# Kernel optimization log

Measured on AMD Instinct MI355X. Metric: run time of the kernel, lower is better.

## Reference

```python
import jax, jax.numpy as jnp
import numpy as np
import math

M = 0.5
S = 64.0
COS_M = math.cos(M)
SIN_M = math.sin(M)
THRESHOLD = math.cos(math.pi - M)
MM = math.sin(math.pi - M) * M

B, D, N_CLASSES = 512, 512, 100000


def setup_inputs() -> dict:
    key = jax.random.key(0)
    k1, k2, k3 = jax.random.split(key, 3)
    embeddings = jax.random.normal(k1, (B, D), dtype=jnp.float32)
    labels = jax.random.randint(k2, (B,), 0, N_CLASSES, dtype=jnp.int32)
    kernel = jax.random.normal(k3, (D, N_CLASSES), dtype=jnp.float32) * 0.05
    t = jnp.zeros((), dtype=jnp.float32)
    return {"embeddings": embeddings, "labels": labels, "kernel": kernel, "t": t}


def reference(embeddings, labels, kernel, t):
    # L2 normalize embeddings (rows) and kernel (columns)
    emb = embeddings / jnp.linalg.norm(embeddings, axis=1, keepdims=True)
    kn = kernel / jnp.linalg.norm(kernel, axis=0, keepdims=True)
    cos_theta = jnp.clip(emb @ kn, -1.0, 1.0)  # [B, C]

    b = cos_theta.shape[0]
    rows = jnp.arange(b)
    target_logit = cos_theta[rows, labels][:, None]  # [B, 1]
    sin_theta = jnp.sqrt(1.0 - jnp.square(target_logit))
    cos_theta_m = target_logit * COS_M - sin_theta * SIN_M  # [B, 1]

    mask = cos_theta > cos_theta_m  # [B, C] hard examples
    final_target_logit = jnp.where(target_logit > THRESHOLD,
                                   cos_theta_m, target_logit - MM)  # [B, 1]

    # EMA update of t (assigned before the hard-example scaling in TF code)
    new_t = 0.01 * jnp.mean(target_logit) + 0.99 * t

    # hard examples: c -> c * (t + c); others unchanged
    cos_theta = jnp.where(mask, cos_theta * (new_t + cos_theta), cos_theta)
    # overwrite label column with the margin-adjusted target logit
    cos_theta = cos_theta.at[rows, labels].set(final_target_logit[:, 0])
    return cos_theta * S
```

## Files before the change

### kernel.cpp

```cpp
#include <hip/hip_runtime.h>
#include <hip/hip_bf16.h>
#include <cstdint>
#include <cstddef>

#define C_N 100000
#define B_N 512
#define D_N 512

#define COS_M_F   0.87758256189037276f
#define SIN_M_F   0.47942553860420301f
#define THRESH_F  (-0.87758256189037276f)
#define MM_F      0.23971276930210150f
#define S_F       64.0f

typedef __attribute__((ext_vector_type(8))) short short8;
typedef __attribute__((ext_vector_type(4))) float f32x4;

__device__ __forceinline__ unsigned short f2bf(float f) {
  unsigned u = __float_as_uint(f);
  u = u + 0x7fffu + ((u >> 16) & 1u);
  return (unsigned short)(u >> 16);
}

__device__ __forceinline__ float wave_sum(float v) {
#pragma unroll
  for (int o = 32; o > 0; o >>= 1) v += __shfl_down(v, o, 64);
  return v;
}

__device__ __forceinline__ void lds_load16(const void* g, void* l) {
  __builtin_amdgcn_global_load_lds(
      (const __attribute__((address_space(1))) unsigned int*)g,
      (__attribute__((address_space(3))) unsigned int*)l, 16, 0, 0);
}

__launch_bounds__(512)
__global__ void knorm2_k(const float* __restrict__ Kp, float* __restrict__ cninv,
                         unsigned short* __restrict__ Knt) {
  __shared__ __align__(16) unsigned short Tl[64 * 512];
  __shared__ float ssum[32][64];
  __shared__ float cns[64];

  const int t = threadIdx.x;
  const int j0 = blockIdx.x * 64;
  const int jq = t & 15;
  const int dr = t >> 4;
  const int jcol = min((j0 >> 2) + jq, (C_N >> 2) - 1);
  const float4* __restrict__ Kv = (const float4*)Kp;

  float4 v[16];
#pragma unroll
  for (int i = 0; i < 16; ++i)
    v[i] = Kv[(size_t)(dr * 16 + i) * (C_N / 4) + jcol];

  float s0 = 0.f, s1 = 0.f, s2 = 0.f, s3 = 0.f;
#pragma unroll
  for (int i = 0; i < 16; ++i) {
    s0 = fmaf(v[i].x, v[i].x, s0);
    s1 = fmaf(v[i].y, v[i].y, s1);
    s2 = fmaf(v[i].z, v[i].z, s2);
    s3 = fmaf(v[i].w, v[i].w, s3);
  }
  ssum[dr][jq * 4 + 0] = s0;
  ssum[dr][jq * 4 + 1] = s1;
  ssum[dr][jq * 4 + 2] = s2;
  ssum[dr][jq * 4 + 3] = s3;
  __syncthreads();
  if (t < 64) {
    float s = 0.f;
#pragma unroll
    for (int d = 0; d < 32; ++d) s += ssum[d][t];
    float r = rsqrtf(fmaxf(s, 1e-30f));
    cns[t] = r;
    if (j0 + t < C_N) cninv[j0 + t] = r;
  }
  __syncthreads();

  const float r0 = cns[jq * 4 + 0];
  const float r1 = cns[jq * 4 + 1];
  const float r2 = cns[jq * 4 + 2];
  const float r3 = cns[jq * 4 + 3];
#pragma unroll
  for (int g = 0; g < 4; ++g) {
    const int ch = dr * 2 + (g >> 1);
    const int sub = (g & 1) * 8;
#pragma unroll
    for (int c = 0; c < 4; ++c) {
      const int j = jq * 4 + c;
      const float rc = (c == 0) ? r0 : (c == 1) ? r1 : (c == 2) ? r2 : r3;
      unsigned lo, hi;
      lo = (unsigned)f2bf(v[g * 4 + 0][c] * rc) | ((unsigned)f2bf(v[g * 4 + 1][c] * rc) << 16);
      hi = (unsigned)f2bf(v[g * 4 + 2][c] * rc) | ((unsigned)f2bf(v[g * 4 + 3][c] * rc) << 16);
      const int phys = ch ^ (j & 7);
      *(uint2*)((char*)Tl + j * 1024 + phys * 16 + sub) = make_uint2(lo, hi);
    }
  }
  __syncthreads();

  const int jr = t >> 3;
  const int dc = t & 7;
  const int jg = j0 + jr;
  if (jg < C_N) {
#pragma unroll
    for (int s = 0; s < 8; ++s) {
      const int phys = (s * 8) + (dc ^ (jr & 7));
      uint4 val = *(const uint4*)((const char*)Tl + jr * 1024 + phys * 16);
      *(uint4*)(&Knt[(size_t)jg * D_N + s * 64 + dc * 8]) = val;
    }
  }
}

__global__ void embnorm_k(const float* __restrict__ emb, unsigned short* __restrict__ embn,
                          float* __restrict__ rinv) {
  int row = blockIdx.x;
  int t = threadIdx.x;
  float4 v = ((const float4*)(emb + (size_t)row * D_N))[t];
  float ss = v.x * v.x + v.y * v.y + v.z * v.z + v.w * v.w;
  ss = wave_sum(ss);
  __shared__ float red[2];
  if ((t & 63) == 0) red[t >> 6] = ss;
  __syncthreads();
  float tot = red[0] + red[1];
  float ri = rsqrtf(tot);
  if (t == 0) rinv[row] = ri;
  ushort4 o;
  o.x = f2bf(v.x * ri); o.y = f2bf(v.y * ri); o.z = f2bf(v.z * ri); o.w = f2bf(v.w * ri);
  ((ushort4*)(embn + (size_t)row * D_N))[t] = o;
}

__global__ void target2_k(const float* __restrict__ emb, const float* __restrict__ Kp,
                          const float* __restrict__ rinv, const int* __restrict__ labels,
                          float* __restrict__ target, float* __restrict__ ctm,
                          float* __restrict__ ft) {
  int row = blockIdx.x;
  int t = threadIdx.x;
  int lab = labels[row];
  float p = 0.f, ss = 0.f;
  for (int d = t; d < D_N; d += 256) {
    float kv = Kp[(size_t)d * C_N + lab];
    p = fmaf(emb[(size_t)row * D_N + d], kv, p);
    ss = fmaf(kv, kv, ss);
  }
  p = wave_sum(p);
  ss = wave_sum(ss);
  __shared__ float redp[4], reds[4];
  if ((t & 63) == 0) { redp[t >> 6] = p; reds[t >> 6] = ss; }
  __syncthreads();
  if (t == 0) {
    float dot = redp[0] + redp[1] + redp[2] + redp[3];
    float sums = reds[0] + reds[1] + reds[2] + reds[3];
    float tg = dot * rinv[row] * rsqrtf(fmaxf(sums, 1e-30f));
    tg = fminf(fmaxf(tg, -1.f), 1.f);
    float st = sqrtf(fmaxf(1.f - tg * tg, 0.f));
    float cm = tg * COS_M_F - st * SIN_M_F;
    float f = (tg > THRESH_F) ? cm : (tg - MM_F);
    target[row] = tg;
    ctm[row] = cm;
    ft[row] = f;
  }
}

__global__ void newt_k(const float* __restrict__ target, const float* __restrict__ t_in,
                       float* __restrict__ newt) {
  int t = threadIdx.x;
  float v = target[t];
  v = wave_sum(v);
  __shared__ float red[8];
  if ((t & 63) == 0) red[t >> 6] = v;
  __syncthreads();
  if (t == 0) {
    float s = 0.f;
#pragma unroll
    for (int i = 0; i < 8; ++i) s += red[i];
    *newt = 0.01f * (s / (float)B_N) + 0.99f * t_in[0];
  }
}

__launch_bounds__(1024, 4)
__global__ void gemm8_k(const unsigned short* __restrict__ Knt,
                        const unsigned short* __restrict__ embn,
                        const int* __restrict__ labels,
                        const float* __restrict__ ctm, const float* __restrict__ ft,
                        const float* __restrict__ newt_p, float* __restrict__ out) {
  __shared__ __align__(16) char lds[81920];
  unsigned short* Al = (unsigned short*)lds;
  unsigned short* Bb = (unsigned short*)(lds + 65536);

  const int t = threadIdx.x;
  const int l = t & 63, w = t >> 6;
  const int j0 = blockIdx.x * 128;

  const int sidx = (l & 7) ^ (l >> 3);
  const int r0 = ((l >> 3) << 1) | (sidx >> 2);
  const int kc8 = (sidx & 3) * 8;

  const unsigned short* asrc = embn + (size_t)(w * 32 + r0) * D_N + kc8;
  const unsigned short* bsrc = Knt + (size_t)(j0 + (w & 7) * 16 + r0) * D_N + kc8;

#pragma unroll
  for (int p = 0; p < 2; ++p)
    lds_load16(asrc + p * 16 * D_N, Al + w * 1024 + p * 512);
  if (w < 8) lds_load16(bsrc, Bb + w * 512);
  __syncthreads();

  const int wr = w >> 2, wc = w & 3;
  const int lq = l >> 4, lr = l & 15;
  const int s16 = ((((lr & 1) << 2) | lq) ^ (lr >> 1)) << 4;
  const int rh = lr >> 1;

  f32x4 acc[8][2];
#pragma unroll
  for (int mb = 0; mb < 8; ++mb) {
    acc[mb][0] = 0;
    acc[mb][1] = 0;
  }

#pragma unroll
  for (int it = 0; it < 16; ++it) {
    const int cur = it & 1, nxt = cur ^ 1;
    if (it < 15) {
      const int k0 = (it + 1) * 32;
#pragma unroll
      for (int p = 0; p < 2; ++p)
        lds_load16(asrc + p * 16 * D_N + k0, Al + nxt * 16384 + w * 1024 + p * 512);
      if (w < 8) lds_load16(bsrc + k0, Bb + nxt * 4096 + w * 512);
    }
    const char* Ab = (const char*)(Al + cur * 16384);
    const char* Bt = (const char*)(Bb + cur * 4096);
    short8 b0 = *(const short8*)(Bt + ((wc * 16 + 0 + rh) << 7) + s16);
    short8 b1 = *(const short8*)(Bt + ((wc * 16 + 8 + rh) << 7) + s16);
#pragma unroll
    for (int mb = 0; mb < 8; ++mb) {
      short8 a = *(const short8*)(Ab + ((wr * 64 + mb * 8 + rh) << 7) + s16);
      acc[mb][0] = __builtin_amdgcn_mfma_f32_16x16x32_bf16(a, b0, acc[mb][0], 0, 0, 0);
      acc[mb][1] = __builtin_amdgcn_mfma_f32_16x16x32_bf16(a, b1, acc[mb][1], 0, 0, 0);
    }
    __syncthreads();
  }

  const float newt = *newt_p;
  float* Tl = (float*)lds;
  const int row_l = t >> 3;
  const int sgl = t & 7;
  const int rx = row_l & 7;

#pragma unroll
  for (int pp = 0; pp < 4; ++pp) {
    if (wr == pp) {
#pragma unroll
      for (int mb = 0; mb < 8; ++mb) {
#pragma unroll
        for (int nb = 0; nb < 2; ++nb) {
          const int seg = nb * 4 + (lr >> 2);
          const int e = lr & 3;
#pragma unroll
          for (int r = 0; r < 4; ++r) {
            const int rl = mb * 16 + lq * 4 + r;
            const int ps = seg ^ (rl & 7);
            Tl[rl * 128 + wc * 32 + ps * 4 + e] = acc[mb][nb][r];
          }
        }
      }
    }
    __syncthreads();
    const int grow = pp * 128 + row_l;
    const int lab = labels[grow];
    const float cm = ctm[grow];
    const float f = ft[grow];
#pragma unroll
    for (int k = 0; k < 4; ++k) {
      const int jb = j0 + k * 32 + sgl * 4;
      if (jb < C_N) {
        f32x4 vv = *(const f32x4*)&Tl[row_l * 128 + k * 32 + (sgl ^ rx) * 4];
#pragma unroll
        for (int e = 0; e < 4; ++e) {
          float c = fminf(fmaxf(vv[e], -1.f), 1.f);
          float o = (c > cm) ? c * (newt + c) : c;
          o = (jb + e == lab) ? f : o;
          vv[e] = o * S_F;
        }
        *(f32x4*)&out[(size_t)grow * C_N + jb] = vv;
      }
    }
    __syncthreads();
  }
}

extern "C" void kernel_launch(void* const* d_in, const int* in_sizes, int n_in,
                              void* d_out, int out_size, void* d_ws, size_t ws_size,
                              hipStream_t stream) {
  (void)in_sizes; (void)n_in; (void)out_size; (void)ws_size;
  const float* emb = (const float*)d_in[0];
  const int* labels = (const int*)d_in[1];
  const float* Kp = (const float*)d_in[2];
  const float* t_in = (const float*)d_in[3];
  float* out = (float*)d_out;

  char* wsp = (char*)d_ws;
  const size_t KNT_BYTES = (size_t)100096 * D_N * 2;
  unsigned short* Knt = (unsigned short*)(wsp + 0);
  unsigned short* embn = (unsigned short*)(wsp + KNT_BYTES);
  float* cninv  = (float*)(wsp + KNT_BYTES + 524288);
  float* target = (float*)(wsp + KNT_BYTES + 524288 + 400000);
  float* ctm    = (float*)(wsp + KNT_BYTES + 524288 + 400000 + 2048);
  float* ft     = (float*)(wsp + KNT_BYTES + 524288 + 400000 + 2 * 2048);
  float* rinv   = (float*)(wsp + KNT_BYTES + 524288 + 400000 + 3 * 2048);
  float* newt   = (float*)(wsp + KNT_BYTES + 524288 + 400000 + 4 * 2048);

  knorm2_k<<<(C_N + 63) / 64, 512, 0, stream>>>(Kp, cninv, Knt);
  embnorm_k<<<B_N, 128, 0, stream>>>(emb, embn, rinv);
  target2_k<<<B_N, 256, 0, stream>>>(emb, Kp, rinv, labels, target, ctm, ft);
  newt_k<<<1, 512, 0, stream>>>(target, t_in, newt);
  gemm8_k<<<(C_N + 127) / 128, 1024, 0, stream>>>(Knt, embn, labels, ctm, ft, newt, out);
}
```

Measured before the change: 201.2 us.

## Remap GEMM blocks per XCD and pipeline global-to-LDS loads with explicit waitcnts

Block indices are remapped so consecutive column tiles land on the same XCD, which should improve L2 locality for the shared embedding tile. The K loop now issues two stages ahead and replaces __syncthreads with explicit vmcnt/lgkmcnt waits and raw s_barrier, so global loads can overlap MFMA work instead of draining every iteration. It relies on hand-counted outstanding-load counts, which become wrong if lds_load16's instruction count changes.

```diff
diff --git a/kernel.cpp b/kernel.cpp
--- a/kernel.cpp
+++ b/kernel.cpp
@@ -177,7 +177,7 @@
 }
 
 __launch_bounds__(1024, 4)
-__global__ void gemm8_k(const unsigned short* __restrict__ Knt,
+__global__ void gemm9_k(const unsigned short* __restrict__ Knt,
                         const unsigned short* __restrict__ embn,
                         const int* __restrict__ labels,
                         const float* __restrict__ ctm, const float* __restrict__ ft,
@@ -188,7 +188,12 @@
 
   const int t = threadIdx.x;
   const int l = t & 63, w = t >> 6;
-  const int j0 = blockIdx.x * 128;
+
+  const int nwg = gridDim.x;
+  const int q = nwg >> 3, r = nwg & 7;
+  const int xcd = blockIdx.x & 7, seq = blockIdx.x >> 3;
+  const int wg = (xcd < r ? xcd * (q + 1) : r * (q + 1) + (xcd - r) * q) + seq;
+  const int j0 = wg * 128;
 
   const int sidx = (l & 7) ^ (l >> 3);
   const int r0 = ((l >> 3) << 1) | (sidx >> 2);
@@ -197,11 +202,16 @@
   const unsigned short* asrc = embn + (size_t)(w * 32 + r0) * D_N + kc8;
   const unsigned short* bsrc = Knt + (size_t)(j0 + (w & 7) * 16 + r0) * D_N + kc8;
 
-#pragma unroll
-  for (int p = 0; p < 2; ++p)
-    lds_load16(asrc + p * 16 * D_N, Al + w * 1024 + p * 512);
-  if (w < 8) lds_load16(bsrc, Bb + w * 512);
-  __syncthreads();
+#define STAGE9(it, buf)                                                        \
+  do {                                                                         \
+    const int k0_ = (it) * 32;                                                 \
+    lds_load16(asrc + k0_, Al + (buf) * 16384 + w * 1024);                     \
+    lds_load16(asrc + 16 * D_N + k0_, Al + (buf) * 16384 + w * 1024 + 512);    \
+    if (w < 8) lds_load16(bsrc + k0_, Bb + (buf) * 4096 + w * 512);            \
+  } while (0)
+
+  STAGE9(0, 0);
+  STAGE9(1, 1);
 
   const int wr = w >> 2, wc = w & 3;
   const int lq = l >> 4, lr = l & 15;
@@ -217,14 +227,19 @@
 
 #pragma unroll
   for (int it = 0; it < 16; ++it) {
-    const int cur = it & 1, nxt = cur ^ 1;
-    if (it < 15) {
-      const int k0 = (it + 1) * 32;
-#pragma unroll
-      for (int p = 0; p < 2; ++p)
-        lds_load16(asrc + p * 16 * D_N + k0, Al + nxt * 16384 + w * 1024 + p * 512);
-      if (w < 8) lds_load16(bsrc + k0, Bb + nxt * 4096 + w * 512);
-    }
+    const int cur = it & 1;
+    if (it >= 1 && it < 15) STAGE9(it + 1, cur ^ 1);
+    if (it == 15) {
+      asm volatile("s_waitcnt vmcnt(0)" ::: "memory");
+    } else if (w < 8) {
+      asm volatile("s_waitcnt vmcnt(3)" ::: "memory");
+    } else {
+      asm volatile("s_waitcnt vmcnt(2)" ::: "memory");
+    }
+    __builtin_amdgcn_sched_barrier(0);
+    __builtin_amdgcn_s_barrier();
+    __builtin_amdgcn_sched_barrier(0);
+
     const char* Ab = (const char*)(Al + cur * 16384);
     const char* Bt = (const char*)(Bb + cur * 4096);
     short8 b0 = *(const short8*)(Bt + ((wc * 16 + 0 + rh) << 7) + s16);
@@ -235,8 +250,12 @@
       acc[mb][0] = __builtin_amdgcn_mfma_f32_16x16x32_bf16(a, b0, acc[mb][0], 0, 0, 0);
       acc[mb][1] = __builtin_amdgcn_mfma_f32_16x16x32_bf16(a, b1, acc[mb][1], 0, 0, 0);
     }
-    __syncthreads();
-  }
+    asm volatile("s_waitcnt lgkmcnt(0)" ::: "memory");
+    __builtin_amdgcn_sched_barrier(0);
+    __builtin_amdgcn_s_barrier();
+    __builtin_amdgcn_sched_barrier(0);
+  }
+#undef STAGE9
 
   const float newt = *newt_p;
   float* Tl = (float*)lds;
@@ -254,10 +273,10 @@
           const int seg = nb * 4 + (lr >> 2);
           const int e = lr & 3;
 #pragma unroll
-          for (int r = 0; r < 4; ++r) {
-            const int rl = mb * 16 + lq * 4 + r;
+          for (int rr = 0; rr < 4; ++rr) {
+            const int rl = mb * 16 + lq * 4 + rr;
             const int ps = seg ^ (rl & 7);
-            Tl[rl * 128 + wc * 32 + ps * 4 + e] = acc[mb][nb][r];
+            Tl[rl * 128 + wc * 32 + ps * 4 + e] = acc[mb][nb][rr];
           }
         }
       }
@@ -311,5 +330,5 @@
   embnorm_k<<<B_N, 128, 0, stream>>>(emb, embn, rinv);
   target2_k<<<B_N, 256, 0, stream>>>(emb, Kp, rinv, labels, target, ctm, ft);
   newt_k<<<1, 512, 0, stream>>>(target, t_in, newt);
-  gemm8_k<<<(C_N + 127) / 128, 1024, 0, stream>>>(Knt, embn, labels, ctm, ft, newt, out);
-}
+  gemm9_k<<<(C_N + 127) / 128, 1024, 0, stream>>>(Knt, embn, labels, ctm, ft, newt, out);
+}
```

After: 201.9 us. No clear change (+0.4%).

## Retile GEMM to 256x64 blocks with direct epilogue stores

Applied to the files above, without the earlier changes.

Replaces the 1024-thread kernel (512 rows x 128 columns per block) with 256-thread blocks that each cover 256 rows x 64 columns, giving more, smaller blocks with a smaller LDS footprint per block. The epilogue no longer stages results through LDS for coalesced float4 stores. Each lane now writes scalar floats straight from its MFMA accumulators. This drops the LDS transpose and its barriers, but the global stores become strided and scalar, which may hurt write coalescing on a store-bound output. Each embedding tile is also reloaded once per column tile.

```diff
diff --git a/kernel.cpp b/kernel.cpp
--- a/kernel.cpp
+++ b/kernel.cpp
@@ -176,34 +176,36 @@
   }
 }
 
-__launch_bounds__(1024, 4)
-__global__ void gemm8_k(const unsigned short* __restrict__ Knt,
-                        const unsigned short* __restrict__ embn,
-                        const int* __restrict__ labels,
-                        const float* __restrict__ ctm, const float* __restrict__ ft,
-                        const float* __restrict__ newt_p, float* __restrict__ out) {
-  __shared__ __align__(16) char lds[81920];
-  unsigned short* Al = (unsigned short*)lds;
-  unsigned short* Bb = (unsigned short*)(lds + 65536);
+__launch_bounds__(256, 4)
+__global__ void gemm10_k(const unsigned short* __restrict__ Knt,
+                         const unsigned short* __restrict__ embn,
+                         const int* __restrict__ labels,
+                         const float* __restrict__ ctm, const float* __restrict__ ft,
+                         const float* __restrict__ newt_p, float* __restrict__ out) {
+  __shared__ __align__(16) unsigned short Al[2][8192];
+  __shared__ __align__(16) unsigned short Bb[2][2048];
 
   const int t = threadIdx.x;
   const int l = t & 63, w = t >> 6;
-  const int j0 = blockIdx.x * 128;
+  const int mi = blockIdx.x & 1;
+  const int jb = blockIdx.x >> 1;
+  const int m0 = mi * 256;
+  const int j0 = jb * 64;
 
   const int sidx = (l & 7) ^ (l >> 3);
   const int r0 = ((l >> 3) << 1) | (sidx >> 2);
   const int kc8 = (sidx & 3) * 8;
 
-  const unsigned short* asrc = embn + (size_t)(w * 32 + r0) * D_N + kc8;
-  const unsigned short* bsrc = Knt + (size_t)(j0 + (w & 7) * 16 + r0) * D_N + kc8;
-
-#pragma unroll
-  for (int p = 0; p < 2; ++p)
-    lds_load16(asrc + p * 16 * D_N, Al + w * 1024 + p * 512);
-  if (w < 8) lds_load16(bsrc, Bb + w * 512);
-  __syncthreads();
-
-  const int wr = w >> 2, wc = w & 3;
+  const unsigned short* asrc = embn + (size_t)(m0 + w * 64 + r0) * D_N + kc8;
+  const unsigned short* bsrc = Knt + (size_t)(j0 + w * 16 + r0) * D_N + kc8;
+
+#pragma unroll
+  for (int p = 0; p < 4; ++p)
+    lds_load16(asrc + p * 16 * D_N, &Al[0][w * 2048 + p * 512]);
+  lds_load16(bsrc, &Bb[0][w * 512]);
+  __syncthreads();
+
+  const int wr = w >> 1, wc = w & 1;
   const int lq = l >> 4, lr = l & 15;
   const int s16 = ((((lr & 1) << 2) | lq) ^ (lr >> 1)) << 4;
   const int rh = lr >> 1;
@@ -221,12 +223,12 @@
     if (it < 15) {
       const int k0 = (it + 1) * 32;
 #pragma unroll
-      for (int p = 0; p < 2; ++p)
-        lds_load16(asrc + p * 16 * D_N + k0, Al + nxt * 16384 + w * 1024 + p * 512);
-      if (w < 8) lds_load16(bsrc + k0, Bb + nxt * 4096 + w * 512);
-    }
-    const char* Ab = (const char*)(Al + cur * 16384);
-    const char* Bt = (const char*)(Bb + cur * 4096);
+      for (int p = 0; p < 4; ++p)
+        lds_load16(asrc + p * 16 * D_N + k0, &Al[nxt][w * 2048 + p * 512]);
+      lds_load16(bsrc + k0, &Bb[nxt][w * 512]);
+    }
+    const char* Ab = (const char*)Al[cur];
+    const char* Bt = (const char*)Bb[cur];
     short8 b0 = *(const short8*)(Bt + ((wc * 16 + 0 + rh) << 7) + s16);
     short8 b1 = *(const short8*)(Bt + ((wc * 16 + 8 + rh) << 7) + s16);
 #pragma unroll
@@ -239,50 +241,30 @@
   }
 
   const float newt = *newt_p;
-  float* Tl = (float*)lds;
-  const int row_l = t >> 3;
-  const int sgl = t & 7;
-  const int rx = row_l & 7;
-
-#pragma unroll
-  for (int pp = 0; pp < 4; ++pp) {
-    if (wr == pp) {
-#pragma unroll
-      for (int mb = 0; mb < 8; ++mb) {
-#pragma unroll
-        for (int nb = 0; nb < 2; ++nb) {
-          const int seg = nb * 4 + (lr >> 2);
-          const int e = lr & 3;
-#pragma unroll
-          for (int r = 0; r < 4; ++r) {
-            const int rl = mb * 16 + lq * 4 + r;
-            const int ps = seg ^ (rl & 7);
-            Tl[rl * 128 + wc * 32 + ps * 4 + e] = acc[mb][nb][r];
-          }
-        }
+  const int jn0 = j0 + wc * 32 + lr;
+  const int jn1 = jn0 + 16;
+#pragma unroll
+  for (int mb = 0; mb < 8; ++mb) {
+    const int ibase = wr * 128 + mb * 16 + 4 * lq;
+#pragma unroll
+    for (int r = 0; r < 4; ++r) {
+      const int grow = m0 + ibase + r;
+      const int lab = labels[grow];
+      const float cm = ctm[grow];
+      const float f = ft[grow];
+      {
+        float c = fminf(fmaxf(acc[mb][0][r], -1.f), 1.f);
+        float o = (c > cm) ? c * (newt + c) : c;
+        o = (jn0 == lab) ? f : o;
+        if (jn0 < C_N) out[(size_t)grow * C_N + jn0] = o * S_F;
       }
-    }
-    __syncthreads();
-    const int grow = pp * 128 + row_l;
-    const int lab = labels[grow];
-    const float cm = ctm[grow];
-    const float f = ft[grow];
-#pragma unroll
-    for (int k = 0; k < 4; ++k) {
-      const int jb = j0 + k * 32 + sgl * 4;
-      if (jb < C_N) {
-        f32x4 vv = *(const f32x4*)&Tl[row_l * 128 + k * 32 + (sgl ^ rx) * 4];
-#pragma unroll
-        for (int e = 0; e < 4; ++e) {
-          float c = fminf(fmaxf(vv[e], -1.f), 1.f);
-          float o = (c > cm) ? c * (newt + c) : c;
-          o = (jb + e == lab) ? f : o;
-          vv[e] = o * S_F;
-        }
-        *(f32x4*)&out[(size_t)grow * C_N + jb] = vv;
+      {
+        float c = fminf(fmaxf(acc[mb][1][r], -1.f), 1.f);
+        float o = (c > cm) ? c * (newt + c) : c;
+        o = (jn1 == lab) ? f : o;
+        if (jn1 < C_N) out[(size_t)grow * C_N + jn1] = o * S_F;
       }
     }
-    __syncthreads();
   }
 }
 
@@ -311,5 +293,6 @@
   embnorm_k<<<B_N, 128, 0, stream>>>(emb, embn, rinv);
   target2_k<<<B_N, 256, 0, stream>>>(emb, Kp, rinv, labels, target, ctm, ft);
   newt_k<<<1, 512, 0, stream>>>(target, t_in, newt);
-  gemm8_k<<<(C_N + 127) / 128, 1024, 0, stream>>>(Knt, embn, labels, ctm, ft, newt, out);
-}
+  const int jblocks = (C_N + 63) / 64;
+  gemm10_k<<<jblocks * 2, 256, 0, stream>>>(Knt, embn, labels, ctm, ft, newt, out);
+}
```

Result: faster. 194.2 us (-3.5%).
